# Kernel tuning notes

Measured on AMD Instinct MI355X. Metric: run time of the kernel, lower is better.

## Reference

```python
import jax, jax.numpy as jnp
import numpy as np

N, D, H, E, K = 16384, 256, 512, 16, 2  # nodes, node_dim, expert hidden, n_experts, active_k
LB_WEIGHT = 0.01
EPS = 1e-5


def setup_inputs() -> dict:
    key = jax.random.key(0)
    k0, k1, k2, k3 = jax.random.split(key, 4)
    x = jax.random.normal(k0, (N, D), jnp.float32)
    # router weight: torch nn.Linear(D, E, bias=False) -> weight [E, D], init std=0.02
    Wr = jax.random.normal(k1, (E, D), jnp.float32) * 0.02
    # stacked expert weights (torch Linear weights transposed to [in, out])
    W1 = jax.random.normal(k2, (E, D, H), jnp.float32) * 0.02
    W2 = jax.random.normal(k3, (E, H, D), jnp.float32) * 0.02
    ln_gamma = jnp.ones((D,), jnp.float32)
    ln_beta = jnp.zeros((D,), jnp.float32)
    return {"x": x, "Wr": Wr, "W1": W1, "W2": W2, "ln_gamma": ln_gamma, "ln_beta": ln_beta}


def reference(x, Wr, W1, W2, ln_gamma, ln_beta):
    n = x.shape[0]
    router_logits = x @ Wr.T                                  # [N, E]
    router_probs = jax.nn.softmax(router_logits, axis=-1)     # [N, E]
    top_w, top_i = jax.lax.top_k(router_probs, K)             # [N, K] each
    top_w = top_w / (top_w.sum(axis=-1, keepdims=True) + 1e-9)
    # dense combine weights: cw[n, e] = renormalized weight if e selected else 0
    cw = jnp.zeros((n, E), x.dtype).at[jnp.arange(n)[:, None], top_i].set(top_w)
    # per-expert FFN on all tokens (fixed-shape dense dispatch), exact-erf GELU like nn.GELU
    h = jax.nn.gelu(jnp.einsum('nd,edh->neh', x, W1), approximate=False)  # [N, E, H]
    y = jnp.einsum('neh,ehd->ned', h, W2)                     # [N, E, D]
    moe_out = jnp.einsum('ne,ned->nd', cw, y)                 # [N, D]
    # residual + LayerNorm
    z = x + moe_out
    mu = z.mean(axis=-1, keepdims=True)
    var = ((z - mu) ** 2).mean(axis=-1, keepdims=True)
    out = (z - mu) / jnp.sqrt(var + EPS) * ln_gamma + ln_beta
    # load-balance loss (counts are non-differentiable, like torch.no_grad())
    counts = jax.ops.segment_sum(jnp.ones((n * K,), router_probs.dtype),
                                 top_i.reshape(-1), num_segments=E)
    frac_tokens = jax.lax.stop_gradient(counts) / (n * K + 1e-9)
    lb_loss = LB_WEIGHT * (E * jnp.sum(frac_tokens * router_probs.mean(axis=0)))
    return out, lb_loss, jax.lax.stop_gradient(router_probs), top_i
```

## Files before the change

kernel.cpp:

```cpp
#include <hip/hip_runtime.h>
#include <hip/hip_bf16.h>
#include <math.h>

#define N_TOK 16384
#define DIM   256
#define HID   512
#define NEXP  16
#define NSLOT (N_TOK * 2)
#define RT    32
#define MAXT  (NSLOT / RT + NEXP)

typedef __attribute__((ext_vector_type(8))) short bf16x8;
typedef __attribute__((ext_vector_type(4))) float f32x4;
#define MFMA(a, b, c) __builtin_amdgcn_mfma_f32_16x16x32_bf16(a, b, c, 0, 0, 0)

__device__ __forceinline__ unsigned short f2b(float f) {
  union { float f; unsigned int i; } c; c.f = f;
  unsigned int r = c.i + 0x7FFFu + ((c.i >> 16) & 1u);
  return (unsigned short)(r >> 16);
}

__device__ __forceinline__ float gelu_f(float v) {
  float v2 = v * v;
  float u2 = v * fmaf(0.10294322f, v2, 2.3022082f);
  float s  = __builtin_amdgcn_exp2f(u2);
  float r  = __builtin_amdgcn_rcpf(1.0f + s);
  return fmaf(-v, r, v);
}

__global__ __launch_bounds__(256) void prep_kernel(
    const float* __restrict__ W1, const float* __restrict__ W2, const float* __restrict__ x,
    unsigned short* __restrict__ W1f, unsigned short* __restrict__ W2f, unsigned short* __restrict__ xb)
{
  int id = blockIdx.x * 256 + threadIdx.x;
  if (id < 524288) {
    int i4 = id * 4;
    int inner = i4 & 31;
    int h  = (i4 >> 5) & 511;
    int kb = (i4 >> 14) & 7;
    int e  = i4 >> 17;
    const float* src = W1 + ((size_t)(e * 256 + kb * 32 + inner) * 512 + h);
    ushort4 o;
    o.x = f2b(src[0]); o.y = f2b(src[512]); o.z = f2b(src[1024]); o.w = f2b(src[1536]);
    *(ushort4*)(W1f + i4) = o;
  } else if (id < 1048576) {
    int i4 = (id - 524288) * 4;
    int inner = i4 & 31;
    int d2 = (i4 >> 5) & 255;
    int kb = (i4 >> 13) & 15;
    int e  = i4 >> 17;
    const float* src = W2 + ((size_t)(e * 512 + kb * 32 + inner) * 256 + d2);
    ushort4 o;
    o.x = f2b(src[0]); o.y = f2b(src[256]); o.z = f2b(src[512]); o.w = f2b(src[768]);
    *(ushort4*)(W2f + i4) = o;
  } else {
    int j = id - 1048576;
    float4 xv = *(const float4*)(x + (size_t)j * 4);
    ushort4 o;
    o.x = f2b(xv.x); o.y = f2b(xv.y); o.z = f2b(xv.z); o.w = f2b(xv.w);
    *(ushort4*)(xb + (size_t)j * 4) = o;
  }
}

__global__ __launch_bounds__(256) void router_kernel(
    const float* __restrict__ x, const float* __restrict__ Wr,
    float* __restrict__ probs_out, float* __restrict__ topi_out,
    float* __restrict__ topw, int* __restrict__ sel, float* __restrict__ g_partial)
{
  __shared__ float sp[16];
  int tid = threadIdx.x;
  int wv = tid >> 6, lane = tid & 63;
  int tok = blockIdx.x * 4 + wv;
  int e = lane & 15, q = lane >> 4;
  if (tid < 16) sp[tid] = 0.f;
  __syncthreads();

  const float4* xr = (const float4*)(x + (size_t)tok * DIM + q * 64);
  const float4* wr = (const float4*)(Wr + (size_t)e * DIM + q * 64);
  float a0 = 0.f, a1 = 0.f, a2 = 0.f, a3 = 0.f;
  #pragma unroll
  for (int i = 0; i < 16; ++i) {
    float4 xa = xr[i], wa = wr[i];
    a0 += xa.x * wa.x; a1 += xa.y * wa.y; a2 += xa.z * wa.z; a3 += xa.w * wa.w;
  }
  float lg = (a0 + a1) + (a2 + a3);
  lg += __shfl_xor(lg, 16, 64);
  lg += __shfl_xor(lg, 32, 64);

  float mx = lg;
  #pragma unroll
  for (int o = 1; o < 16; o <<= 1) mx = fmaxf(mx, __shfl_xor(mx, o, 64));
  float ex = expf(lg - mx);
  float ssum = ex;
  #pragma unroll
  for (int o = 1; o < 16; o <<= 1) ssum += __shfl_xor(ssum, o, 64);
  float p = ex / ssum;

  if (lane < 16) {
    probs_out[(size_t)tok * NEXP + e] = p;
    atomicAdd(&sp[e], p);
  }

  float p1 = p; int i1 = e;
  #pragma unroll
  for (int o = 1; o < 16; o <<= 1) {
    float po = __shfl_xor(p1, o, 64); int io = __shfl_xor(i1, o, 64);
    if (po > p1 || (po == p1 && io < i1)) { p1 = po; i1 = io; }
  }
  float pm = (e == i1) ? -1.f : p;
  float p2 = pm; int i2 = e;
  #pragma unroll
  for (int o = 1; o < 16; o <<= 1) {
    float po = __shfl_xor(p2, o, 64); int io = __shfl_xor(i2, o, 64);
    if (po > p2 || (po == p2 && io < i2)) { p2 = po; i2 = io; }
  }
  if (lane == 0) {
    float rs = 1.0f / (p1 + p2 + 1e-9f);
    int s0 = tok * 2;
    topw[s0] = p1 * rs;  topw[s0 + 1] = p2 * rs;
    sel[s0] = i1;        sel[s0 + 1] = i2;
    topi_out[s0] = (float)i1;  topi_out[s0 + 1] = (float)i2;
  }
  __syncthreads();
  if (tid < 16) g_partial[(size_t)tid * 4096 + blockIdx.x] = sp[tid];
}

__global__ __launch_bounds__(256) void scatter_kernel(
    const int* __restrict__ sel, const float* __restrict__ topw,
    int* __restrict__ cursors, int* __restrict__ tok_of_pos, float* __restrict__ w_of_pos)
{
  __shared__ int bcnt[16];
  __shared__ int bbase[16];
  int tid = threadIdx.x;
  if (tid < 16) bcnt[tid] = 0;
  __syncthreads();
  int s = blockIdx.x * 256 + tid;
  int e = sel[s];
  int my = atomicAdd(&bcnt[e], 1);
  __syncthreads();
  if (tid < 16) bbase[tid] = atomicAdd(&cursors[tid], bcnt[tid]);
  __syncthreads();
  int idx = e * NSLOT + bbase[e] + my;
  tok_of_pos[idx] = s >> 1;
  w_of_pos[idx]   = topw[s];
}

__global__ __launch_bounds__(1024) void stats_kernel(
    const int* __restrict__ cursors, const float* __restrict__ g_partial,
    int* __restrict__ perm, float* __restrict__ lb_out)
{
  __shared__ float sp[16];
  int tid = threadIdx.x;
  int wv = tid >> 6, lane = tid & 63;
  float sacc = 0.f;
  #pragma unroll
  for (int j = 0; j < 64; ++j) sacc += g_partial[(size_t)wv * 4096 + j * 64 + lane];
  #pragma unroll
  for (int o = 32; o; o >>= 1) sacc += __shfl_xor(sacc, o, 64);
  if (lane == 0) sp[wv] = sacc;
  __syncthreads();

  if (tid == 0) {
    float acc = 0.f;
    for (int e = 0; e < NEXP; ++e)
      acc += ((float)cursors[e] / (32768.0f + 1e-9f)) * (sp[e] * (1.0f / 16384.0f));
    lb_out[0] = 0.01f * 16.0f * acc;
    int pos = 0;
    for (int g = 0; g < 8; ++g)
      for (int h = 0; h < 2; ++h) {
        int e = g + h * 8;
        int nt = (cursors[e] + RT - 1) / RT;
        for (int mt = 0; mt < nt; ++mt) perm[pos++] = (e << 16) | mt;
      }
    for (; pos < MAXT; ++pos) perm[pos] = -1;
  }
}

__global__ __launch_bounds__(256, 3) void ffn_kernel(
    const unsigned short* __restrict__ xb,
    const unsigned short* __restrict__ W1f, const unsigned short* __restrict__ W2f,
    const int* __restrict__ cursors, const int* __restrict__ perm,
    const int* __restrict__ tok_of_pos, const float* __restrict__ w_of_pos,
    float* __restrict__ zbuf)
{
  __shared__ __align__(16) unsigned short As[8 * 32 * 32];
  __shared__ __align__(16) unsigned short Hs[16 * 32 * 32];
  __shared__ float rwS[RT];
  __shared__ int   tokS[RT];

  int b = blockIdx.x;
  int rr = (b & 7) * (MAXT / 8) + (b >> 3);
  int pv = perm[rr];
  if (pv < 0) return;
  int e = pv >> 16, mtile = pv & 0xFFFF;
  int cnt = cursors[e];
  int base = e * NSLOT;
  int m0 = mtile * RT;

  int tid = threadIdx.x;
  if (tid < RT) {
    int rl = m0 + tid;
    tokS[tid] = (rl < cnt) ? tok_of_pos[base + rl] : -1;
    rwS[tid]  = (rl < cnt) ? w_of_pos[base + rl] : 0.f;
  }
  __syncthreads();

  {
    int cb = tid & 31;
    int r0 = tid >> 5;
    int lo = (cb >> 2) * 1024 + (cb & 3) * 8;
    #pragma unroll
    for (int q = 0; q < 4; ++q) {
      int row = r0 + q * 8;
      int tk = tokS[row];
      bf16x8 v = {0, 0, 0, 0, 0, 0, 0, 0};
      if (tk >= 0) v = *(const bf16x8*)(xb + (size_t)tk * DIM + cb * 8);
      *(bf16x8*)&As[lo + row * 32] = v;
    }
  }
  __syncthreads();

  int lane = tid & 63;
  int w = tid >> 6;
  int l15 = lane & 15, g = lane >> 4;

  bf16x8 af[2][8];
  #pragma unroll
  for (int mf = 0; mf < 2; ++mf)
    #pragma unroll
    for (int kb = 0; kb < 8; ++kb)
      af[mf][kb] = *(bf16x8*)&As[kb * 1024 + (mf * 16 + l15) * 32 + g * 8];

  const unsigned short* W1e = W1f + (size_t)e * (8 * 512 * 32);
  #pragma unroll
  for (int cf = 0; cf < 8; ++cf) {
    int col0 = w * 128 + cf * 16;
    f32x4 ac0 = {0.f, 0.f, 0.f, 0.f}, ac1 = {0.f, 0.f, 0.f, 0.f};
    #pragma unroll
    for (int kb = 0; kb < 8; ++kb) {
      bf16x8 bfr = *(const bf16x8*)(W1e + (size_t)(kb * 512 + col0 + l15) * 32 + g * 8);
      ac0 = MFMA(af[0][kb], bfr, ac0);
      ac1 = MFMA(af[1][kb], bfr, ac1);
    }
    int col = col0 + l15;
    int kbo = (col >> 5) * 1024 + (col & 31);
    #pragma unroll
    for (int reg = 0; reg < 4; ++reg) {
      int row0 = g * 4 + reg;
      Hs[kbo + row0 * 32]        = f2b(gelu_f(ac0[reg]));
      Hs[kbo + (row0 + 16) * 32] = f2b(gelu_f(ac1[reg]));
    }
  }
  __syncthreads();

  const unsigned short* W2e = W2f + (size_t)e * (16 * 256 * 32);
  #pragma unroll
  for (int mf = 0; mf < 2; ++mf) {
    bf16x8 hf[16];
    #pragma unroll
    for (int kb = 0; kb < 16; ++kb)
      hf[kb] = *(bf16x8*)&Hs[kb * 1024 + (mf * 16 + l15) * 32 + g * 8];

    f32x4 ac[4];
    #pragma unroll
    for (int cf = 0; cf < 4; ++cf) ac[cf] = (f32x4){0.f, 0.f, 0.f, 0.f};

    #pragma unroll
    for (int kb = 0; kb < 16; ++kb) {
      #pragma unroll
      for (int cf = 0; cf < 4; ++cf) {
        bf16x8 bfr = *(const bf16x8*)(W2e + (size_t)(kb * 256 + w * 64 + cf * 16 + l15) * 32 + g * 8);
        ac[cf] = MFMA(hf[kb], bfr, ac[cf]);
      }
    }

    #pragma unroll
    for (int cf = 0; cf < 4; ++cf) {
      int col = w * 64 + cf * 16 + l15;
      #pragma unroll
      for (int reg = 0; reg < 4; ++reg) {
        int row = mf * 16 + g * 4 + reg;
        int t = tokS[row];
        if (t >= 0) atomicAdd(zbuf + (size_t)t * DIM + col, ac[cf][reg] * rwS[row]);
      }
    }
  }
}

__global__ __launch_bounds__(256) void combine_ln_kernel(
    const float* __restrict__ x, const float* __restrict__ zbuf,
    const float* __restrict__ gamma, const float* __restrict__ beta,
    float* __restrict__ outp)
{
  int wv = threadIdx.x >> 6, lane = threadIdx.x & 63;
  int tok = blockIdx.x * 4 + wv;
  int d0 = lane << 2;
  float4 xv = *(const float4*)(x + (size_t)tok * DIM + d0);
  float4 mv = *(const float4*)(zbuf + (size_t)tok * DIM + d0);
  float z0 = xv.x + mv.x, z1 = xv.y + mv.y, z2 = xv.z + mv.z, z3 = xv.w + mv.w;
  float s = z0 + z1 + z2 + z3;
  float q = z0 * z0 + z1 * z1 + z2 * z2 + z3 * z3;
  #pragma unroll
  for (int off = 32; off > 0; off >>= 1) {
    s += __shfl_xor(s, off, 64);
    q += __shfl_xor(q, off, 64);
  }
  float mu  = s * (1.0f / 256.0f);
  float var = q * (1.0f / 256.0f) - mu * mu;
  float inv = rsqrtf(var + 1e-5f);
  float4 gv = *(const float4*)(gamma + d0);
  float4 bv = *(const float4*)(beta + d0);
  float4 ov;
  ov.x = (z0 - mu) * inv * gv.x + bv.x;
  ov.y = (z1 - mu) * inv * gv.y + bv.y;
  ov.z = (z2 - mu) * inv * gv.z + bv.z;
  ov.w = (z3 - mu) * inv * gv.w + bv.w;
  *(float4*)(outp + (size_t)tok * DIM + d0) = ov;
}

extern "C" void kernel_launch(void* const* d_in, const int* in_sizes, int n_in,
                              void* d_out, int out_size, void* d_ws, size_t ws_size,
                              hipStream_t stream)
{
  const float* x     = (const float*)d_in[0];
  const float* Wr    = (const float*)d_in[1];
  const float* W1    = (const float*)d_in[2];
  const float* W2    = (const float*)d_in[3];
  const float* gamma = (const float*)d_in[4];
  const float* beta  = (const float*)d_in[5];

  float* ob = (float*)d_out;
  float* out_main  = ob;
  float* lb_out    = ob + (size_t)N_TOK * DIM;
  float* probs_out = ob + (size_t)N_TOK * DIM + 1;
  float* topi_out  = ob + (size_t)N_TOK * DIM + 1 + (size_t)N_TOK * NEXP;

  char* ws = (char*)d_ws;
  int*   cursors    = (int*)(ws + 0);
  int*   perm       = (int*)(ws + 1024);
  float* g_partial  = (float*)(ws + 65536);
  float* topw       = (float*)(ws + 327680);
  int*   sel        = (int*)(ws + 458752);
  int*   tok_of_pos = (int*)(ws + 589824);
  float* w_of_pos   = (float*)(ws + 2686976);
  unsigned short* xb  = (unsigned short*)(ws + 4980736);
  unsigned short* W1f = (unsigned short*)(ws + 13369344);
  unsigned short* W2f = (unsigned short*)(ws + 17563648);
  float* zbuf       = (float*)(ws + 21757952);

  hipMemsetAsync(cursors, 0, 64, stream);
  hipMemsetAsync(zbuf, 0, (size_t)N_TOK * DIM * 4, stream);
  prep_kernel<<<8192, 256, 0, stream>>>(W1, W2, x, W1f, W2f, xb);
  router_kernel<<<N_TOK / 4, 256, 0, stream>>>(x, Wr, probs_out, topi_out, topw, sel, g_partial);
  scatter_kernel<<<NSLOT / 256, 256, 0, stream>>>(sel, topw, cursors, tok_of_pos, w_of_pos);
  stats_kernel<<<1, 1024, 0, stream>>>(cursors, g_partial, perm, lb_out);
  ffn_kernel<<<MAXT, 256, 0, stream>>>(xb, W1f, W2f, cursors, perm, tok_of_pos, w_of_pos, zbuf);
  combine_ln_kernel<<<N_TOK / 4, 256, 0, stream>>>(x, zbuf, gamma, beta, out_main);
}
```

Baseline: 240.1 us.

## Fuse x bf16 cast into router, parallelize perm build, widen FFN blocks to 512 threads

The x-to-bf16 conversion moves from the prep kernel into the router kernel, which already reads x, so x is not read a second time. The stats kernel now builds the tile permutation with all threads from per-group prefix offsets, replacing a serial single-thread loop. The FFN kernel runs 8 waves per block instead of 4, splitting columns finer. In the second GEMM each wave holds its W2 fragments in registers and streams H from shared memory, which changes register pressure and the pattern of shared-memory traffic.

```diff
diff --git a/kernel.cpp b/kernel.cpp
--- a/kernel.cpp
+++ b/kernel.cpp
@@ -29,8 +29,8 @@
 }
 
 __global__ __launch_bounds__(256) void prep_kernel(
-    const float* __restrict__ W1, const float* __restrict__ W2, const float* __restrict__ x,
-    unsigned short* __restrict__ W1f, unsigned short* __restrict__ W2f, unsigned short* __restrict__ xb)
+    const float* __restrict__ W1, const float* __restrict__ W2,
+    unsigned short* __restrict__ W1f, unsigned short* __restrict__ W2f)
 {
   int id = blockIdx.x * 256 + threadIdx.x;
   if (id < 524288) {
@@ -43,7 +43,7 @@
     ushort4 o;
     o.x = f2b(src[0]); o.y = f2b(src[512]); o.z = f2b(src[1024]); o.w = f2b(src[1536]);
     *(ushort4*)(W1f + i4) = o;
-  } else if (id < 1048576) {
+  } else {
     int i4 = (id - 524288) * 4;
     int inner = i4 & 31;
     int d2 = (i4 >> 5) & 255;
@@ -53,19 +53,14 @@
     ushort4 o;
     o.x = f2b(src[0]); o.y = f2b(src[256]); o.z = f2b(src[512]); o.w = f2b(src[768]);
     *(ushort4*)(W2f + i4) = o;
-  } else {
-    int j = id - 1048576;
-    float4 xv = *(const float4*)(x + (size_t)j * 4);
-    ushort4 o;
-    o.x = f2b(xv.x); o.y = f2b(xv.y); o.z = f2b(xv.z); o.w = f2b(xv.w);
-    *(ushort4*)(xb + (size_t)j * 4) = o;
   }
 }
 
 __global__ __launch_bounds__(256) void router_kernel(
     const float* __restrict__ x, const float* __restrict__ Wr,
     float* __restrict__ probs_out, float* __restrict__ topi_out,
-    float* __restrict__ topw, int* __restrict__ sel, float* __restrict__ g_partial)
+    float* __restrict__ topw, int* __restrict__ sel, float* __restrict__ g_partial,
+    unsigned short* __restrict__ xb)
 {
   __shared__ float sp[16];
   int tid = threadIdx.x;
@@ -101,6 +96,13 @@
     atomicAdd(&sp[e], p);
   }
 
+  {
+    float4 xc = *(const float4*)(x + (size_t)tok * DIM + lane * 4);
+    ushort4 o;
+    o.x = f2b(xc.x); o.y = f2b(xc.y); o.z = f2b(xc.z); o.w = f2b(xc.w);
+    *(ushort4*)(xb + (size_t)tok * DIM + lane * 4) = o;
+  }
+
   float p1 = p; int i1 = e;
   #pragma unroll
   for (int o = 1; o < 16; o <<= 1) {
@@ -150,6 +152,8 @@
     int* __restrict__ perm, float* __restrict__ lb_out)
 {
   __shared__ float sp[16];
+  __shared__ int nt[16];
+  __shared__ int P[9];
   int tid = threadIdx.x;
   int wv = tid >> 6, lane = tid & 63;
   float sacc = 0.f;
@@ -158,6 +162,7 @@
   #pragma unroll
   for (int o = 32; o; o >>= 1) sacc += __shfl_xor(sacc, o, 64);
   if (lane == 0) sp[wv] = sacc;
+  if (tid < 16) nt[tid] = (cursors[tid] + RT - 1) / RT;
   __syncthreads();
 
   if (tid == 0) {
@@ -165,18 +170,28 @@
     for (int e = 0; e < NEXP; ++e)
       acc += ((float)cursors[e] / (32768.0f + 1e-9f)) * (sp[e] * (1.0f / 16384.0f));
     lb_out[0] = 0.01f * 16.0f * acc;
-    int pos = 0;
-    for (int g = 0; g < 8; ++g)
-      for (int h = 0; h < 2; ++h) {
-        int e = g + h * 8;
-        int nt = (cursors[e] + RT - 1) / RT;
-        for (int mt = 0; mt < nt; ++mt) perm[pos++] = (e << 16) | mt;
-      }
-    for (; pos < MAXT; ++pos) perm[pos] = -1;
-  }
-}
-
-__global__ __launch_bounds__(256, 3) void ffn_kernel(
+    int pp = 0;
+    for (int g = 0; g < 8; ++g) { P[g] = pp; pp += nt[g] + nt[g + 8]; }
+    P[8] = pp;
+  }
+  __syncthreads();
+
+  for (int t = tid; t < MAXT; t += 1024) {
+    int g = 0;
+    #pragma unroll
+    for (int gg = 1; gg < 8; ++gg) if (t >= P[gg]) g = gg;
+    int v = -1;
+    if (t < P[8]) {
+      int r = t - P[g];
+      int e = (r < nt[g]) ? g : g + 8;
+      int mt = (r < nt[g]) ? r : r - nt[g];
+      v = (e << 16) | mt;
+    }
+    perm[t] = v;
+  }
+}
+
+__global__ __launch_bounds__(512, 4) void ffn_kernel(
     const unsigned short* __restrict__ xb,
     const unsigned short* __restrict__ W1f, const unsigned short* __restrict__ W2f,
     const int* __restrict__ cursors, const int* __restrict__ perm,
@@ -205,18 +220,14 @@
   }
   __syncthreads();
 
-  {
-    int cb = tid & 31;
-    int r0 = tid >> 5;
-    int lo = (cb >> 2) * 1024 + (cb & 3) * 8;
-    #pragma unroll
-    for (int q = 0; q < 4; ++q) {
-      int row = r0 + q * 8;
-      int tk = tokS[row];
-      bf16x8 v = {0, 0, 0, 0, 0, 0, 0, 0};
-      if (tk >= 0) v = *(const bf16x8*)(xb + (size_t)tk * DIM + cb * 8);
-      *(bf16x8*)&As[lo + row * 32] = v;
-    }
+  #pragma unroll
+  for (int q = 0; q < 2; ++q) {
+    int idx = q * 512 + tid;
+    int row = idx >> 5, cb = idx & 31;
+    int tk = tokS[row];
+    bf16x8 v = {0, 0, 0, 0, 0, 0, 0, 0};
+    if (tk >= 0) v = *(const bf16x8*)(xb + (size_t)tk * DIM + cb * 8);
+    *(bf16x8*)&As[(cb >> 2) * 1024 + (cb & 3) * 8 + row * 32] = v;
   }
   __syncthreads();
 
@@ -233,8 +244,8 @@
 
   const unsigned short* W1e = W1f + (size_t)e * (8 * 512 * 32);
   #pragma unroll
-  for (int cf = 0; cf < 8; ++cf) {
-    int col0 = w * 128 + cf * 16;
+  for (int cf = 0; cf < 4; ++cf) {
+    int col0 = w * 64 + cf * 16;
     f32x4 ac0 = {0.f, 0.f, 0.f, 0.f}, ac1 = {0.f, 0.f, 0.f, 0.f};
     #pragma unroll
     for (int kb = 0; kb < 8; ++kb) {
@@ -255,33 +266,27 @@
 
   const unsigned short* W2e = W2f + (size_t)e * (16 * 256 * 32);
   #pragma unroll
-  for (int mf = 0; mf < 2; ++mf) {
-    bf16x8 hf[16];
+  for (int cf = 0; cf < 2; ++cf) {
+    int col0 = w * 32 + cf * 16;
+    bf16x8 bfr[16];
     #pragma unroll
     for (int kb = 0; kb < 16; ++kb)
-      hf[kb] = *(bf16x8*)&Hs[kb * 1024 + (mf * 16 + l15) * 32 + g * 8];
-
-    f32x4 ac[4];
-    #pragma unroll
-    for (int cf = 0; cf < 4; ++cf) ac[cf] = (f32x4){0.f, 0.f, 0.f, 0.f};
-
-    #pragma unroll
-    for (int kb = 0; kb < 16; ++kb) {
+      bfr[kb] = *(const bf16x8*)(W2e + (size_t)(kb * 256 + col0 + l15) * 32 + g * 8);
+
+    #pragma unroll
+    for (int mf = 0; mf < 2; ++mf) {
+      f32x4 ac = {0.f, 0.f, 0.f, 0.f};
       #pragma unroll
-      for (int cf = 0; cf < 4; ++cf) {
-        bf16x8 bfr = *(const bf16x8*)(W2e + (size_t)(kb * 256 + w * 64 + cf * 16 + l15) * 32 + g * 8);
-        ac[cf] = MFMA(hf[kb], bfr, ac[cf]);
+      for (int kb = 0; kb < 16; ++kb) {
+        bf16x8 hfr = *(bf16x8*)&Hs[kb * 1024 + (mf * 16 + l15) * 32 + g * 8];
+        ac = MFMA(hfr, bfr[kb], ac);
       }
-    }
-
-    #pragma unroll
-    for (int cf = 0; cf < 4; ++cf) {
-      int col = w * 64 + cf * 16 + l15;
+      int col = col0 + l15;
       #pragma unroll
       for (int reg = 0; reg < 4; ++reg) {
         int row = mf * 16 + g * 4 + reg;
         int t = tokS[row];
-        if (t >= 0) atomicAdd(zbuf + (size_t)t * DIM + col, ac[cf][reg] * rwS[row]);
+        if (t >= 0) atomicAdd(zbuf + (size_t)t * DIM + col, ac[reg] * rwS[row]);
       }
     }
   }
@@ -350,10 +355,10 @@
 
   hipMemsetAsync(cursors, 0, 64, stream);
   hipMemsetAsync(zbuf, 0, (size_t)N_TOK * DIM * 4, stream);
-  prep_kernel<<<8192, 256, 0, stream>>>(W1, W2, x, W1f, W2f, xb);
-  router_kernel<<<N_TOK / 4, 256, 0, stream>>>(x, Wr, probs_out, topi_out, topw, sel, g_partial);
+  prep_kernel<<<4096, 256, 0, stream>>>(W1, W2, W1f, W2f);
+  router_kernel<<<N_TOK / 4, 256, 0, stream>>>(x, Wr, probs_out, topi_out, topw, sel, g_partial, xb);
   scatter_kernel<<<NSLOT / 256, 256, 0, stream>>>(sel, topw, cursors, tok_of_pos, w_of_pos);
   stats_kernel<<<1, 1024, 0, stream>>>(cursors, g_partial, perm, lb_out);
-  ffn_kernel<<<MAXT, 256, 0, stream>>>(xb, W1f, W2f, cursors, perm, tok_of_pos, w_of_pos, zbuf);
+  ffn_kernel<<<MAXT, 512, 0, stream>>>(xb, W1f, W2f, cursors, perm, tok_of_pos, w_of_pos, zbuf);
   combine_ln_kernel<<<N_TOK / 4, 256, 0, stream>>>(x, zbuf, gamma, beta, out_main);
 }
```

Measured after the change: 243.2 us. Within noise of the previous version (+1.3%).
